# Kernel optimization log

Hardware: AMD Instinct MI355X
Metric: run time of the kernel (lower is better)

The kernel has to match this reference:

```python
import jax, jax.numpy as jnp
import numpy as np

N, H = 8192, 128  # nodes, hidden_dim


def setup_inputs() -> dict:
    key = jax.random.key(0)
    ks = jax.random.split(key, 5)
    X = jax.random.normal(ks[0], (N, H), dtype=jnp.float32)
    adj = jax.random.uniform(ks[1], (N, N), dtype=jnp.float32)
    W1 = jax.random.normal(ks[2], (H, H), dtype=jnp.float32) / np.sqrt(H).astype(np.float32)
    b1 = jnp.zeros((H,), jnp.float32)
    W2 = jax.random.normal(ks[3], (H, H), dtype=jnp.float32) / np.sqrt(H).astype(np.float32)
    b2 = jnp.zeros((H,), jnp.float32)
    a = jax.random.normal(ks[4], (2 * H, 1), dtype=jnp.float32) * 0.1
    return {"X": X, "adj": adj, "W1": W1, "b1": b1, "W2": W2, "b2": b2, "a": a}


def reference(X, adj, W1, b1, W2, b2, a):
    n = X.shape[0]
    leaky = jax.nn.leaky_relu  # negative_slope = 0.01, matches torch defaults

    # --- GCN diffusion: A_hat = A + I, symmetric normalization, 3 hops ---
    A_hat = adj + jnp.eye(n, dtype=adj.dtype)
    dinv_sqrt = jax.lax.rsqrt(A_hat.sum(axis=1))
    A_norm = dinv_sqrt[:, None] * A_hat * dinv_sqrt[None, :]
    hA = A_norm @ X
    hA2 = A_norm @ hA
    hA3 = A_norm @ hA2
    hA, hA2, hA3 = leaky(hA), leaky(hA2), leaky(hA3)

    # --- scattering diffusion: lazy walk P = 0.5*(I + A D^-1), wavelets ---
    deg = adj.sum(axis=1)
    AD = adj / deg[None, :]  # A @ D^{-1} (column-normalized)

    def P(v):
        return 0.5 * (v + AD @ v)

    px = P(X)
    p2x = P(px)
    p3x = P(p2x)
    p4x = P(p3x)
    # moment = 1 -> |.|**1
    s1 = jnp.abs(X - px)      # Psi_1 = I - P
    s2 = jnp.abs(px - p2x)    # Psi_2 = P - P^2
    s3 = jnp.abs(p2x - p4x)   # Psi_3 = P^2 - P^4

    # --- 6-way attention fusion ---
    h_all = jnp.stack([hA, hA2, hA3, s1, s2, s3], axis=1)         # [N,6,H]
    h_rep = jnp.broadcast_to(X[:, None, :], h_all.shape)          # [N,6,H]
    a_input = jnp.concatenate([h_rep, h_all], axis=-1)            # [N,6,2H]
    e = jnp.einsum('nsk,ko->ns', jax.nn.relu(a_input), a)         # [N,6]
    attn = jax.nn.softmax(e, axis=1)                              # [N,6]
    h_prime = jnp.mean(attn[:, :, None] * h_all, axis=1)          # [N,H]

    # --- output MLP (Withgres=False, so gres layer is skipped) ---
    out = leaky(h_prime @ W1.T + b1)
    out = leaky(out @ W2.T + b2)
    return out
```

## Files before the change

### kernel.cpp

```cpp
#include <hip/hip_runtime.h>

typedef unsigned short ushort_t;
typedef unsigned int   uint_t;
typedef int   i32x4 __attribute__((ext_vector_type(4)));

typedef __attribute__((address_space(3))) void lds_void_t;
typedef __attribute__((address_space(1))) void gbl_void_t;

#define NN 8192
#define HH 128
#define KS 8
#define KLEN 1024
#define NTQ 16

__device__ __forceinline__ ushort_t f2bf(float x) {
    uint_t u = __float_as_uint(x);
    u += 0x7fffu + ((u >> 16) & 1u);
    return (ushort_t)(u >> 16);
}
__device__ __forceinline__ float bf2f(uint_t lo16) { return __uint_as_float(lo16 << 16); }
__device__ __forceinline__ float leaky(float x) { return x > 0.f ? x : 0.01f * x; }

__global__ __launch_bounds__(256) void conv_rowsum(const float* __restrict__ adj,
    char* __restrict__ adjq, float* __restrict__ s, float* __restrict__ rinv)
{
    const int i = blockIdx.x;
    const float4* arow = (const float4*)(adj + ((size_t)i << 13));
    uint_t* brow = (uint_t*)(adjq + ((size_t)i << 13));
    float partial = 0.f;
    for (int t = threadIdx.x; t < 2048; t += 256) {
        const float4 v = arow[t];
        partial += (v.x + v.y) + (v.z + v.w);
        const uint_t q0 = (uint_t)__float2int_rn(v.x * 127.f);
        const uint_t q1 = (uint_t)__float2int_rn(v.y * 127.f);
        const uint_t q2 = (uint_t)__float2int_rn(v.z * 127.f);
        const uint_t q3 = (uint_t)__float2int_rn(v.w * 127.f);
        brow[t] = q0 | (q1 << 8) | (q2 << 16) | (q3 << 24);
    }
    #pragma unroll
    for (int off = 32; off; off >>= 1) partial += __shfl_xor(partial, off);
    __shared__ float ps[4];
    if ((threadIdx.x & 63) == 0) ps[threadIdx.x >> 6] = partial;
    __syncthreads();
    if (threadIdx.x == 0) {
        const float tot = (ps[0] + ps[1]) + (ps[2] + ps[3]);
        s[i]    = rsqrtf(tot + 1.0f);
        rinv[i] = 1.0f / tot;
    }
}

__global__ __launch_bounds__(256) void preMax(const float* __restrict__ u,
    const float* __restrict__ v, const float* __restrict__ s, const float* __restrict__ rinv,
    float* __restrict__ cmax)
{
    const int j0 = (blockIdx.x & 127) << 6;
    const int c0 = (blockIdx.x >> 7) << 6;
    __shared__ uint_t cm[64];
    if (threadIdx.x < 64) cm[threadIdx.x] = 0;
    __syncthreads();
    const int tx = threadIdx.x & 63;
    const int ty = threadIdx.x >> 6;
    float m = 0.f;
    #pragma unroll
    for (int rr = 0; rr < 16; ++rr) {
        const int j = j0 + ty + (rr << 2);
        const int c = c0 + tx;
        const float val = (c < 128) ? s[j] * u[((size_t)j << 7) + c]
                                    : rinv[j] * v[((size_t)j << 7) + (c - 128)];
        m = fmaxf(m, fabsf(val));
    }
    atomicMax(&cm[tx], __float_as_uint(m));
    __syncthreads();
    if (threadIdx.x < 64)
        atomicMax((uint_t*)&cmax[c0 + threadIdx.x], cm[threadIdx.x]);
}

__global__ __launch_bounds__(256) void preQ(const float* __restrict__ u,
    const float* __restrict__ v, const float* __restrict__ s, const float* __restrict__ rinv,
    const float* __restrict__ cmax, char* __restrict__ Bi8, float* __restrict__ dq)
{
    const int j0 = (blockIdx.x & 127) << 6;
    const int c0 = (blockIdx.x >> 7) << 6;
    __shared__ float tile[64][65];
    const int tx = threadIdx.x & 63;
    const int ty = threadIdx.x >> 6;
    #pragma unroll
    for (int rr = 0; rr < 16; ++rr) {
        const int jl = ty + (rr << 2);
        const int j = j0 + jl;
        const int c = c0 + tx;
        tile[jl][tx] = (c < 128) ? s[j] * u[((size_t)j << 7) + c]
                                 : rinv[j] * v[((size_t)j << 7) + (c - 128)];
    }
    __syncthreads();
    const int cl = threadIdx.x & 63;
    const int jq = threadIdx.x >> 6;
    const float cmv = cmax[c0 + cl];
    const float rs = cmv > 0.f ? 127.f / cmv : 0.f;
    uint_t w4[4];
    #pragma unroll
    for (int g = 0; g < 4; ++g) {
        uint_t wv = 0;
        #pragma unroll
        for (int b = 0; b < 4; ++b) {
            int q = __float2int_rn(tile[(jq << 4) + (g << 2) + b][cl] * rs);
            q = q > 127 ? 127 : (q < -127 ? -127 : q);
            wv |= ((uint_t)(q & 0xff)) << (8 * b);
        }
        w4[g] = wv;
    }
    uint4 st; st.x = w4[0]; st.y = w4[1]; st.z = w4[2]; st.w = w4[3];
    *(uint4*)(Bi8 + ((size_t)(c0 + cl) << 13) + j0 + (jq << 4)) = st;
    if ((blockIdx.x & 127) == 0 && threadIdx.x < 64)
        dq[c0 + threadIdx.x] = cmax[c0 + threadIdx.x] * (1.f / 16129.f);
}

#define WAITB(S) do {                                         \
    asm volatile("s_waitcnt " S ::: "memory");                \
    __builtin_amdgcn_sched_barrier(0);                        \
    __builtin_amdgcn_s_barrier();                             \
    __builtin_amdgcn_sched_barrier(0);                        \
} while (0)

__global__ __launch_bounds__(512, 2) void gemm_i8(const char* __restrict__ A,
    const char* __restrict__ Bt, ushort_t* __restrict__ Yb)
{
    __shared__ char lds[4 * 32768];
    const int bid = blockIdx.x;
    const int mb = bid & 31;
    const int ks = bid >> 5;
    const size_t mBase = (size_t)mb * 256;
    const int tid = threadIdx.x;
    const int w = tid >> 6, l = tid & 63;
    const int wr = w >> 2, wc = w & 3;
    const int frow = l & 15, fk = l >> 4;
    const int fsl = ((fk ^ ((frow >> 1) & 3)) << 4);
    const int srow = l >> 2;
    const int skoff = (((l & 3) ^ ((l >> 3) & 3)) << 4);
    const int kBeg = ks << 10;

    i32x4 acc[8][4] = {};

    auto STAGE = [&](int t) {
        const int k0 = kBeg + (t << 6);
        char* base = &lds[(t & 3) << 15];
        #pragma unroll
        for (int q = 0; q < 2; ++q) {
            const int c = (w << 1) + q;
            const int row = (c << 4) + srow;
            __builtin_amdgcn_global_load_lds(
                (const gbl_void_t*)(A + ((mBase + row) << 13) + k0 + skoff),
                (lds_void_t*)(base + (c << 10)), 16, 0, 0);
            __builtin_amdgcn_global_load_lds(
                (const gbl_void_t*)(Bt + ((size_t)row << 13) + k0 + skoff),
                (lds_void_t*)(base + 16384 + (c << 10)), 16, 0, 0);
        }
    };
    auto COMPUTE = [&](int T) {
        const char* buf = &lds[(T & 3) << 15];
        i32x4 av[8], bv[4];
        #pragma unroll
        for (int mi = 0; mi < 8; ++mi) {
            const int row = (wr << 7) + (mi << 4) + frow;
            av[mi] = *(const i32x4*)(buf + (row << 6) + fsl);
        }
        #pragma unroll
        for (int ni = 0; ni < 4; ++ni) {
            const int col = (wc << 6) + (ni << 4) + frow;
            bv[ni] = *(const i32x4*)(buf + 16384 + (col << 6) + fsl);
        }
        __builtin_amdgcn_s_setprio(1);
        #pragma unroll
        for (int mi = 0; mi < 8; ++mi)
            #pragma unroll
            for (int ni = 0; ni < 4; ++ni)
                acc[mi][ni] = __builtin_amdgcn_mfma_i32_16x16x64_i8(
                    av[mi], bv[ni], acc[mi][ni], 0, 0, 0);
        __builtin_amdgcn_s_setprio(0);
    };

    STAGE(0); STAGE(1); STAGE(2);
    #pragma unroll 1
    for (int T = 0; T < NTQ - 3; ++T) {
        WAITB("vmcnt(8)");
        STAGE(T + 3);
        COMPUTE(T);
    }
    WAITB("vmcnt(8)"); COMPUTE(NTQ - 3);
    WAITB("vmcnt(4)"); COMPUTE(NTQ - 2);
    WAITB("vmcnt(0)"); COMPUTE(NTQ - 1);
    __syncthreads();

    ushort_t* Cs = (ushort_t*)lds;
    const int orow = (l >> 4) << 2;
    const int ocol = l & 15;
    #pragma unroll
    for (int mi = 0; mi < 8; ++mi) {
        #pragma unroll
        for (int ni = 0; ni < 4; ++ni) {
            const int rl = (wr << 7) + (mi << 4) + orow;
            const int cl = (wc << 6) + (ni << 4) + ocol;
            #pragma unroll
            for (int r = 0; r < 4; ++r)
                Cs[(rl + r) * 256 + cl] = f2bf((float)acc[mi][ni][r]);
        }
    }
    __syncthreads();
    const size_t sliceBase = ((size_t)ks * NN + mBase) * 256;
    #pragma unroll
    for (int p = 0; p < 16; ++p) {
        const int idx16 = (p << 9) + tid;
        const int row   = idx16 >> 5;
        const int c16   = idx16 & 31;
        const uint4 v = *(const uint4*)(&Cs[(row << 8) + (c16 << 3)]);
        *(uint4*)(Yb + sliceBase + (size_t)row * 256 + (c16 << 3)) = v;
    }
}

__global__ __launch_bounds__(256, 2) void gemm_half_i8(const char* __restrict__ A,
    const char* __restrict__ Bt, ushort_t* __restrict__ Yb, int nbOff, int nbCount)
{
    __shared__ char lds[2 * 24576];
    const int bid  = blockIdx.x;
    const int mb   = bid & 31;
    const int rest = bid >> 5;
    const int nb   = nbOff + (rest % nbCount);
    const int ks   = rest / nbCount;
    const size_t mBase = (size_t)mb * 256;
    const size_t nBase = (size_t)nb * 128;
    const int tid = threadIdx.x;
    const int w = tid >> 6, l = tid & 63;
    const int wr = w >> 1, wc = w & 1;
    const int frow = l & 15, fk = l >> 4;
    const int fsl = ((fk ^ ((frow >> 1) & 3)) << 4);
    const int srow = l >> 2;
    const int skoff = (((l & 3) ^ ((l >> 3) & 3)) << 4);
    const int kBeg = ks << 10;

    i32x4 acc[8][4] = {};

    auto STAGE = [&](int t) {
        const int k0 = kBeg + (t << 6);
        char* base = &lds[(t & 1) * 24576];
        #pragma unroll
        for (int q = 0; q < 4; ++q) {
            const int c = (w << 2) + q;
            const int row = (c << 4) + srow;
            __builtin_amdgcn_global_load_lds(
                (const gbl_void_t*)(A + ((mBase + row) << 13) + k0 + skoff),
                (lds_void_t*)(base + (c << 10)), 16, 0, 0);
        }
        #pragma unroll
        for (int q = 0; q < 2; ++q) {
            const int c = (w << 1) + q;
            const int row = (c << 4) + srow;
            __builtin_amdgcn_global_load_lds(
                (const gbl_void_t*)(Bt + ((nBase + row) << 13) + k0 + skoff),
                (lds_void_t*)(base + 16384 + (c << 10)), 16, 0, 0);
        }
    };

    STAGE(0);
    __syncthreads();
    #pragma unroll 1
    for (int T = 0; T < NTQ; ++T) {
        if (T + 1 < NTQ) STAGE(T + 1);
        const char* buf = &lds[(T & 1) * 24576];
        i32x4 av[8], bv[4];
        #pragma unroll
        for (int mi = 0; mi < 8; ++mi) {
            const int row = (wr << 7) + (mi << 4) + frow;
            av[mi] = *(const i32x4*)(buf + (row << 6) + fsl);
        }
        #pragma unroll
        for (int ni = 0; ni < 4; ++ni) {
            const int col = (wc << 6) + (ni << 4) + frow;
            bv[ni] = *(const i32x4*)(buf + 16384 + (col << 6) + fsl);
        }
        __builtin_amdgcn_s_setprio(1);
        #pragma unroll
        for (int mi = 0; mi < 8; ++mi)
            #pragma unroll
            for (int ni = 0; ni < 4; ++ni)
                acc[mi][ni] = __builtin_amdgcn_mfma_i32_16x16x64_i8(
                    av[mi], bv[ni], acc[mi][ni], 0, 0, 0);
        __builtin_amdgcn_s_setprio(0);
        __syncthreads();
    }

    const int orow = (l >> 4) << 2;
    const int ocol = l & 15;
    const size_t sliceBase = ((size_t)ks * NN + mBase) * 256 + nBase;
    #pragma unroll
    for (int p = 0; p < 2; ++p) {
        __syncthreads();
        ushort_t* Cs = (ushort_t*)lds;
        #pragma unroll
        for (int mi = 0; mi < 4; ++mi) {
            #pragma unroll
            for (int ni = 0; ni < 4; ++ni) {
                const int rl = (wr << 6) + (mi << 4) + orow;
                const int cl = (wc << 6) + (ni << 4) + ocol;
                #pragma unroll
                for (int r = 0; r < 4; ++r)
                    Cs[(rl + r) * 128 + cl] = f2bf((float)acc[(p << 2) + mi][ni][r]);
            }
        }
        __syncthreads();
        #pragma unroll
        for (int pp = 0; pp < 8; ++pp) {
            const int idx16 = (pp << 8) + tid;
            const int lrow  = idx16 >> 4;
            const int c16   = idx16 & 15;
            const int rowIn = ((lrow >> 6) << 7) + (p << 6) + (lrow & 63);
            const uint4 v = *(const uint4*)(&Cs[(lrow << 7) + (c16 << 3)]);
            *(uint4*)(Yb + sliceBase + (size_t)rowIn * 256 + (c16 << 3)) = v;
        }
    }
}

__global__ __launch_bounds__(256) void reduce_post(const ushort_t* __restrict__ Yb,
    const float* __restrict__ u, const float* __restrict__ v,
    const float* __restrict__ s, const float* __restrict__ rinv,
    float* __restrict__ hop_out, float* __restrict__ walk_out,
    const float* __restrict__ dq, float* __restrict__ cmaxN, int c0Off)
{
    const int j0 = (blockIdx.x & 127) << 6;
    const int c0 = ((blockIdx.x >> 7) + c0Off) << 6;
    const bool hop = (c0 < 128);
    if (hop && hop_out == nullptr) return;
    __shared__ uint_t cm[64];
    if (cmaxN && threadIdx.x < 64) cm[threadIdx.x] = 0;
    if (cmaxN) __syncthreads();
    const int cg = threadIdx.x & 15;
    const int jr = threadIdx.x >> 4;
    const size_t SL = (size_t)NN * 256;
    const float4 dqv = ((const float4*)dq)[(c0 >> 2) + cg];
    float lm0 = 0.f, lm1 = 0.f, lm2 = 0.f, lm3 = 0.f;
    #pragma unroll
    for (int it = 0; it < 4; ++it) {
        const int jl = jr + (it << 4);
        const int j  = j0 + jl;
        const int c  = c0 + (cg << 2);
        const ushort_t* p = Yb + ((size_t)j << 8) + c;
        float e0 = 0.f, e1 = 0.f, e2 = 0.f, e3 = 0.f;
        #pragma unroll
        for (int kss = 0; kss < KS; ++kss) {
            const uint2 q = *(const uint2*)(p + kss * SL);
            e0 += bf2f(q.x & 0xffffu);
            e1 += __uint_as_float(q.x & 0xffff0000u);
            e2 += bf2f(q.y & 0xffffu);
            e3 += __uint_as_float(q.y & 0xffff0000u);
        }
        e0 *= dqv.x; e1 *= dqv.y; e2 *= dqv.z; e3 *= dqv.w;
        float4 o; float scale;
        if (hop) {
            const float si = s[j], si2 = si * si;
            const float4 uu = ((const float4*)u)[((size_t)j << 5) + (c >> 2)];
            o.x = si * e0 + si2 * uu.x;  o.y = si * e1 + si2 * uu.y;
            o.z = si * e2 + si2 * uu.z;  o.w = si * e3 + si2 * uu.w;
            ((float4*)hop_out)[((size_t)j << 5) + (c >> 2)] = o;
            scale = si;
        } else {
            const int cw = c - 128;
            const float4 vv = ((const float4*)v)[((size_t)j << 5) + (cw >> 2)];
            o.x = 0.5f * (vv.x + e0);  o.y = 0.5f * (vv.y + e1);
            o.z = 0.5f * (vv.z + e2);  o.w = 0.5f * (vv.w + e3);
            ((float4*)walk_out)[((size_t)j << 5) + (cw >> 2)] = o;
            scale = rinv[j];
        }
        if (cmaxN) {
            lm0 = fmaxf(lm0, fabsf(scale * o.x));
            lm1 = fmaxf(lm1, fabsf(scale * o.y));
            lm2 = fmaxf(lm2, fabsf(scale * o.z));
            lm3 = fmaxf(lm3, fabsf(scale * o.w));
        }
    }
    if (cmaxN) {
        atomicMax(&cm[(cg << 2) + 0], __float_as_uint(lm0));
        atomicMax(&cm[(cg << 2) + 1], __float_as_uint(lm1));
        atomicMax(&cm[(cg << 2) + 2], __float_as_uint(lm2));
        atomicMax(&cm[(cg << 2) + 3], __float_as_uint(lm3));
        __syncthreads();
        if (threadIdx.x < 64)
            atomicMax((uint_t*)&cmaxN[c0 + threadIdx.x], cm[threadIdx.x]);
    }
}

__global__ __launch_bounds__(256) void fuse_attn(const float* __restrict__ X,
    const float* __restrict__ hA, const float* __restrict__ hA2, const float* __restrict__ hA3,
    const float* __restrict__ px, const float* __restrict__ p2x, const float* __restrict__ p4x,
    const float* __restrict__ a, float* __restrict__ hp)
{
    const int w = threadIdx.x >> 6, l = threadIdx.x & 63;
    const size_t i = (size_t)blockIdx.x * 4 + w;
    const size_t base = i << 7;
    float f[6][2];
    float e[6] = {0.f, 0.f, 0.f, 0.f, 0.f, 0.f};
    #pragma unroll
    for (int h = 0; h < 2; ++h) {
        const int k = l + (h << 6);
        const float a2 = a[128 + k];
        const float x   = X[base + k];
        const float t1  = leaky(hA [base + k]);
        const float t2  = leaky(hA2[base + k]);
        const float t3  = leaky(hA3[base + k]);
        const float pk  = px [base + k];
        const float p2k = p2x[base + k];
        const float p4k = p4x[base + k];
        const float s1 = fabsf(x - pk);
        const float s2 = fabsf(pk - p2k);
        const float s3 = fabsf(p2k - p4k);
        f[0][h] = t1; f[1][h] = t2; f[2][h] = t3;
        f[3][h] = s1; f[4][h] = s2; f[5][h] = s3;
        e[0] += fmaxf(t1, 0.f) * a2;
        e[1] += fmaxf(t2, 0.f) * a2;
        e[2] += fmaxf(t3, 0.f) * a2;
        e[3] += s1 * a2;
        e[4] += s2 * a2;
        e[5] += s3 * a2;
    }
    #pragma unroll
    for (int ss = 0; ss < 6; ++ss) {
        #pragma unroll
        for (int off = 32; off; off >>= 1) e[ss] += __shfl_xor(e[ss], off);
    }
    float mx = e[0];
    #pragma unroll
    for (int ss = 1; ss < 6; ++ss) mx = fmaxf(mx, e[ss]);
    float at[6], sum = 0.f;
    #pragma unroll
    for (int ss = 0; ss < 6; ++ss) { at[ss] = expf(e[ss] - mx); sum += at[ss]; }
    const float inv = 1.f / (6.f * sum);
    #pragma unroll
    for (int h = 0; h < 2; ++h) {
        float o = 0.f;
        #pragma unroll
        for (int ss = 0; ss < 6; ++ss) o += at[ss] * f[ss][h];
        hp[base + l + (h << 6)] = o * inv;
    }
}

__global__ __launch_bounds__(256) void mlp(const float* __restrict__ Hm,
    const float* __restrict__ W, const float* __restrict__ b, float* __restrict__ out)
{
    __shared__ float Ws[128 * 140];
    __shared__ float Hs[16 * 140];
    const int node0 = blockIdx.x << 4;
    for (int rr = 0; rr < 64; ++rr) {
        const int idx = rr * 256 + threadIdx.x;
        Ws[(idx >> 7) * 140 + (idx & 127)] = W[idx];
    }
    #pragma unroll
    for (int rr = 0; rr < 8; ++rr) {
        const int idx = rr * 256 + threadIdx.x;
        Hs[(idx >> 7) * 140 + (idx & 127)] = Hm[((size_t)node0 << 7) + idx];
    }
    __syncthreads();
    const int c = threadIdx.x & 15;
    const int n = threadIdx.x >> 4;
    float acc[8] = {};
    for (int k4 = 0; k4 < 32; ++k4) {
        const float4 h4 = *(const float4*)(&Hs[n * 140 + (k4 << 2)]);
        #pragma unroll
        for (int r = 0; r < 8; ++r) {
            const float4 w4 = *(const float4*)(&Ws[(c + (r << 4)) * 140 + (k4 << 2)]);
            acc[r] += h4.x * w4.x + h4.y * w4.y + h4.z * w4.z + h4.w * w4.w;
        }
    }
    const size_t obase = ((size_t)(node0 + n)) << 7;
    #pragma unroll
    for (int r = 0; r < 8; ++r) {
        const int o = c + (r << 4);
        out[obase + o] = leaky(acc[r] + b[o]);
    }
}

extern "C" void kernel_launch(void* const* d_in, const int* in_sizes, int n_in,
                              void* d_out, int out_size, void* d_ws, size_t ws_size,
                              hipStream_t stream)
{
    const float* X   = (const float*)d_in[0];
    const float* adj = (const float*)d_in[1];
    const float* W1  = (const float*)d_in[2];
    const float* b1  = (const float*)d_in[3];
    const float* W2  = (const float*)d_in[4];
    const float* b2  = (const float*)d_in[5];
    const float* a   = (const float*)d_in[6];
    float* out = (float*)d_out;

    char* ws = (char*)d_ws;
    char*     adjq = ws;
    char*     Bi8  = ws + 67108864ull;
    ushort_t* Yb   = (ushort_t*)(ws + 69206016ull);
    float* hA  = (float*)(ws + 102760448ull);
    float* hA2 = hA  + 1048576;
    float* hA3 = hA2 + 1048576;
    float* px  = hA3 + 1048576;
    float* p2x = px  + 1048576;
    float* p3x = p2x + 1048576;
    float* p4x = p3x + 1048576;
    float* sbuf  = p4x + 1048576;
    float* rinvb = sbuf + 8192;
    float* cmaxb = rinvb + 8192;
    float* dq    = cmaxb + 1024;
    float* cmax1 = cmaxb, *cmax2 = cmaxb + 256, *cmax3 = cmaxb + 512, *cmax4 = cmaxb + 768;
    float* hp   = (float*)Yb;
    float* out1 = (float*)(ws + 69206016ull + 4194304ull);

    hipMemsetAsync(cmaxb, 0, 4096, stream);
    conv_rowsum<<<8192, 256, 0, stream>>>(adj, adjq, sbuf, rinvb);

    preMax<<<512, 256, 0, stream>>>(X, X, sbuf, rinvb, cmax1);
    preQ  <<<512, 256, 0, stream>>>(X, X, sbuf, rinvb, cmax1, Bi8, dq);
    gemm_i8<<<256, 512, 0, stream>>>(adjq, Bi8, Yb);
    reduce_post<<<512, 256, 0, stream>>>(Yb, X, X, sbuf, rinvb,
                                         hA, px, dq, cmax2, 0);
    preQ  <<<512, 256, 0, stream>>>(hA, px, sbuf, rinvb, cmax2, Bi8, dq);
    gemm_i8<<<256, 512, 0, stream>>>(adjq, Bi8, Yb);
    reduce_post<<<512, 256, 0, stream>>>(Yb, hA, px, sbuf, rinvb,
                                         hA2, p2x, dq, cmax3, 0);
    preQ  <<<512, 256, 0, stream>>>(hA2, p2x, sbuf, rinvb, cmax3, Bi8, dq);
    gemm_i8<<<256, 512, 0, stream>>>(adjq, Bi8, Yb);
    reduce_post<<<512, 256, 0, stream>>>(Yb, hA2, p2x, sbuf, rinvb,
                                         hA3, p3x, dq, cmax4, 0);
    preQ  <<<512, 256, 0, stream>>>(hA3, p3x, sbuf, rinvb, cmax4, Bi8, dq);
    gemm_half_i8<<<256, 256, 0, stream>>>(adjq, Bi8, Yb, 1, 1);
    reduce_post<<<256, 256, 0, stream>>>(Yb, nullptr, p3x, sbuf, rinvb,
                                         nullptr, p4x, dq, nullptr, 2);

    fuse_attn<<<2048, 256, 0, stream>>>(X, hA, hA2, hA3, px, p2x, p4x, a, hp);
    mlp<<<512, 256, 0, stream>>>(hp, W1, b1, out1);
    mlp<<<512, 256, 0, stream>>>(out1, W2, b2, out);
}
```

Before: 267.2 us.

## Fuse quantization into reduce via grid barrier and merge attention with MLP

Merges the column-max and quantize passes into one kernel using a software grid barrier, so each reduce step also quantizes the next GEMM's operand in place. Fuses the attention-fusion kernel with both MLP layers into one kernel that keeps intermediates in shared memory. Replaces the memset by zeroing inside conv_rowsum. This removes several kernel launches and global round-trips of activations. The grid barrier depends on all 512 blocks being co-resident, which risks deadlock if occupancy is insufficient, and it makes reduceQuant read dq and write the next dq through the same buffer.

```diff
diff --git a/kernel.cpp b/kernel.cpp
--- a/kernel.cpp
+++ b/kernel.cpp
@@ -12,6 +12,7 @@
 #define KS 8
 #define KLEN 1024
 #define NTQ 16
+#define NBAR 512u
 
 __device__ __forceinline__ ushort_t f2bf(float x) {
     uint_t u = __float_as_uint(x);
@@ -21,10 +22,31 @@
 __device__ __forceinline__ float bf2f(uint_t lo16) { return __uint_as_float(lo16 << 16); }
 __device__ __forceinline__ float leaky(float x) { return x > 0.f ? x : 0.01f * x; }
 
+__device__ __forceinline__ void grid_barrier(uint_t* ctr) {
+    __threadfence();
+    __syncthreads();
+    if (threadIdx.x == 0) {
+        __hip_atomic_fetch_add(ctr, 1u, __ATOMIC_ACQ_REL, __HIP_MEMORY_SCOPE_AGENT);
+        while (__hip_atomic_load(ctr, __ATOMIC_ACQUIRE, __HIP_MEMORY_SCOPE_AGENT) < NBAR)
+            __builtin_amdgcn_s_sleep(2);
+    }
+    __syncthreads();
+}
+__device__ __forceinline__ float cmax_read(const float* p) {
+    return __uint_as_float(__hip_atomic_load((const uint_t*)p,
+        __ATOMIC_RELAXED, __HIP_MEMORY_SCOPE_AGENT));
+}
+
 __global__ __launch_bounds__(256) void conv_rowsum(const float* __restrict__ adj,
-    char* __restrict__ adjq, float* __restrict__ s, float* __restrict__ rinv)
+    char* __restrict__ adjq, float* __restrict__ s, float* __restrict__ rinv,
+    float* __restrict__ zbase)
 {
     const int i = blockIdx.x;
+    if (i == 0) {
+        const float4 z{0.f, 0.f, 0.f, 0.f};
+        ((float4*)zbase)[threadIdx.x] = z;
+        if (threadIdx.x < 128) ((float4*)zbase)[256 + threadIdx.x] = z;
+    }
     const float4* arow = (const float4*)(adj + ((size_t)i << 13));
     uint_t* brow = (uint_t*)(adjq + ((size_t)i << 13));
     float partial = 0.f;
@@ -49,53 +71,36 @@
     }
 }
 
-__global__ __launch_bounds__(256) void preMax(const float* __restrict__ u,
-    const float* __restrict__ v, const float* __restrict__ s, const float* __restrict__ rinv,
-    float* __restrict__ cmax)
-{
-    const int j0 = (blockIdx.x & 127) << 6;
-    const int c0 = (blockIdx.x >> 7) << 6;
-    __shared__ uint_t cm[64];
-    if (threadIdx.x < 64) cm[threadIdx.x] = 0;
-    __syncthreads();
-    const int tx = threadIdx.x & 63;
-    const int ty = threadIdx.x >> 6;
-    float m = 0.f;
-    #pragma unroll
-    for (int rr = 0; rr < 16; ++rr) {
-        const int j = j0 + ty + (rr << 2);
-        const int c = c0 + tx;
-        const float val = (c < 128) ? s[j] * u[((size_t)j << 7) + c]
-                                    : rinv[j] * v[((size_t)j << 7) + (c - 128)];
-        m = fmaxf(m, fabsf(val));
-    }
-    atomicMax(&cm[tx], __float_as_uint(m));
-    __syncthreads();
-    if (threadIdx.x < 64)
-        atomicMax((uint_t*)&cmax[c0 + threadIdx.x], cm[threadIdx.x]);
-}
-
-__global__ __launch_bounds__(256) void preQ(const float* __restrict__ u,
-    const float* __restrict__ v, const float* __restrict__ s, const float* __restrict__ rinv,
-    const float* __restrict__ cmax, char* __restrict__ Bi8, float* __restrict__ dq)
+__global__ __launch_bounds__(256) void quantX(const float* __restrict__ X,
+    const float* __restrict__ s, const float* __restrict__ rinv,
+    float* __restrict__ cmax, char* __restrict__ Bi8, float* __restrict__ dq,
+    uint_t* __restrict__ ctr)
 {
     const int j0 = (blockIdx.x & 127) << 6;
     const int c0 = (blockIdx.x >> 7) << 6;
     __shared__ float tile[64][65];
-    const int tx = threadIdx.x & 63;
-    const int ty = threadIdx.x >> 6;
+    __shared__ uint_t cm[64];
+    const int tid = threadIdx.x;
+    if (tid < 64) cm[tid] = 0;
+    __syncthreads();
+    const int tx = tid & 63, ty = tid >> 6;
+    float m = 0.f;
     #pragma unroll
     for (int rr = 0; rr < 16; ++rr) {
         const int jl = ty + (rr << 2);
         const int j = j0 + jl;
         const int c = c0 + tx;
-        tile[jl][tx] = (c < 128) ? s[j] * u[((size_t)j << 7) + c]
-                                 : rinv[j] * v[((size_t)j << 7) + (c - 128)];
-    }
-    __syncthreads();
-    const int cl = threadIdx.x & 63;
-    const int jq = threadIdx.x >> 6;
-    const float cmv = cmax[c0 + cl];
+        const float val = (c < 128) ? s[j] * X[((size_t)j << 7) + c]
+                                    : rinv[j] * X[((size_t)j << 7) + (c - 128)];
+        tile[jl][tx] = val;
+        m = fmaxf(m, fabsf(val));
+    }
+    atomicMax(&cm[tx], __float_as_uint(m));
+    __syncthreads();
+    if (tid < 64) atomicMax((uint_t*)&cmax[c0 + tid], cm[tid]);
+    grid_barrier(ctr);
+    const int cl = tid & 63, jq = tid >> 6;
+    const float cmv = cmax_read(&cmax[c0 + cl]);
     const float rs = cmv > 0.f ? 127.f / cmv : 0.f;
     uint_t w4[4];
     #pragma unroll
@@ -111,8 +116,8 @@
     }
     uint4 st; st.x = w4[0]; st.y = w4[1]; st.z = w4[2]; st.w = w4[3];
     *(uint4*)(Bi8 + ((size_t)(c0 + cl) << 13) + j0 + (jq << 4)) = st;
-    if ((blockIdx.x & 127) == 0 && threadIdx.x < 64)
-        dq[c0 + threadIdx.x] = cmax[c0 + threadIdx.x] * (1.f / 16129.f);
+    if ((blockIdx.x & 127) == 0 && tid < 64)
+        dq[c0 + tid] = cmv * (1.f / 16129.f);
 }
 
 #define WAITB(S) do {                                         \
@@ -319,21 +324,22 @@
     }
 }
 
-__global__ __launch_bounds__(256) void reduce_post(const ushort_t* __restrict__ Yb,
+__global__ __launch_bounds__(256) void reduceQuant(const ushort_t* __restrict__ Yb,
     const float* __restrict__ u, const float* __restrict__ v,
     const float* __restrict__ s, const float* __restrict__ rinv,
     float* __restrict__ hop_out, float* __restrict__ walk_out,
-    const float* __restrict__ dq, float* __restrict__ cmaxN, int c0Off)
+    const float* __restrict__ dq, float* __restrict__ cmaxN,
+    char* __restrict__ Bi8, float* __restrict__ dqN, uint_t* __restrict__ ctr)
 {
     const int j0 = (blockIdx.x & 127) << 6;
-    const int c0 = ((blockIdx.x >> 7) + c0Off) << 6;
+    const int c0 = (blockIdx.x >> 7) << 6;
     const bool hop = (c0 < 128);
-    if (hop && hop_out == nullptr) return;
+    __shared__ float tile[64][65];
     __shared__ uint_t cm[64];
-    if (cmaxN && threadIdx.x < 64) cm[threadIdx.x] = 0;
-    if (cmaxN) __syncthreads();
-    const int cg = threadIdx.x & 15;
-    const int jr = threadIdx.x >> 4;
+    const int tid = threadIdx.x;
+    if (tid < 64) cm[tid] = 0;
+    __syncthreads();
+    const int cg = tid & 15, jr = tid >> 4;
     const size_t SL = (size_t)NN * 256;
     const float4 dqv = ((const float4*)dq)[(c0 >> 2) + cg];
     float lm0 = 0.f, lm1 = 0.f, lm2 = 0.f, lm3 = 0.f;
@@ -369,37 +375,97 @@
             ((float4*)walk_out)[((size_t)j << 5) + (cw >> 2)] = o;
             scale = rinv[j];
         }
-        if (cmaxN) {
-            lm0 = fmaxf(lm0, fabsf(scale * o.x));
-            lm1 = fmaxf(lm1, fabsf(scale * o.y));
-            lm2 = fmaxf(lm2, fabsf(scale * o.z));
-            lm3 = fmaxf(lm3, fabsf(scale * o.w));
-        }
-    }
-    if (cmaxN) {
-        atomicMax(&cm[(cg << 2) + 0], __float_as_uint(lm0));
-        atomicMax(&cm[(cg << 2) + 1], __float_as_uint(lm1));
-        atomicMax(&cm[(cg << 2) + 2], __float_as_uint(lm2));
-        atomicMax(&cm[(cg << 2) + 3], __float_as_uint(lm3));
-        __syncthreads();
-        if (threadIdx.x < 64)
-            atomicMax((uint_t*)&cmaxN[c0 + threadIdx.x], cm[threadIdx.x]);
-    }
-}
-
-__global__ __launch_bounds__(256) void fuse_attn(const float* __restrict__ X,
+        const float b0 = scale * o.x, b1 = scale * o.y;
+        const float b2 = scale * o.z, b3 = scale * o.w;
+        const int clb = cg << 2;
+        tile[jl][clb + 0] = b0;  tile[jl][clb + 1] = b1;
+        tile[jl][clb + 2] = b2;  tile[jl][clb + 3] = b3;
+        lm0 = fmaxf(lm0, fabsf(b0));  lm1 = fmaxf(lm1, fabsf(b1));
+        lm2 = fmaxf(lm2, fabsf(b2));  lm3 = fmaxf(lm3, fabsf(b3));
+    }
+    atomicMax(&cm[(cg << 2) + 0], __float_as_uint(lm0));
+    atomicMax(&cm[(cg << 2) + 1], __float_as_uint(lm1));
+    atomicMax(&cm[(cg << 2) + 2], __float_as_uint(lm2));
+    atomicMax(&cm[(cg << 2) + 3], __float_as_uint(lm3));
+    __syncthreads();
+    if (tid < 64) atomicMax((uint_t*)&cmaxN[c0 + tid], cm[tid]);
+    grid_barrier(ctr);
+    const int cl = tid & 63, jq = tid >> 6;
+    const float cmv = cmax_read(&cmaxN[c0 + cl]);
+    const float rs = cmv > 0.f ? 127.f / cmv : 0.f;
+    uint_t w4[4];
+    #pragma unroll
+    for (int g = 0; g < 4; ++g) {
+        uint_t wv = 0;
+        #pragma unroll
+        for (int b = 0; b < 4; ++b) {
+            int q = __float2int_rn(tile[(jq << 4) + (g << 2) + b][cl] * rs);
+            q = q > 127 ? 127 : (q < -127 ? -127 : q);
+            wv |= ((uint_t)(q & 0xff)) << (8 * b);
+        }
+        w4[g] = wv;
+    }
+    uint4 st; st.x = w4[0]; st.y = w4[1]; st.z = w4[2]; st.w = w4[3];
+    *(uint4*)(Bi8 + ((size_t)(c0 + cl) << 13) + j0 + (jq << 4)) = st;
+    if ((blockIdx.x & 127) == 0 && tid < 64)
+        dqN[c0 + tid] = cmv * (1.f / 16129.f);
+}
+
+__global__ __launch_bounds__(256) void reduce4(const ushort_t* __restrict__ Yb,
+    const float* __restrict__ v, const float* __restrict__ dq,
+    float* __restrict__ walk_out)
+{
+    const int j0 = (blockIdx.x & 127) << 6;
+    const int c0 = ((blockIdx.x >> 7) + 2) << 6;
+    const int cg = threadIdx.x & 15, jr = threadIdx.x >> 4;
+    const size_t SL = (size_t)NN * 256;
+    const float4 dqv = ((const float4*)dq)[(c0 >> 2) + cg];
+    #pragma unroll
+    for (int it = 0; it < 4; ++it) {
+        const int jl = jr + (it << 4);
+        const int j  = j0 + jl;
+        const int c  = c0 + (cg << 2);
+        const ushort_t* p = Yb + ((size_t)j << 8) + c;
+        float e0 = 0.f, e1 = 0.f, e2 = 0.f, e3 = 0.f;
+        #pragma unroll
+        for (int kss = 0; kss < KS; ++kss) {
+            const uint2 q = *(const uint2*)(p + kss * SL);
+            e0 += bf2f(q.x & 0xffffu);
+            e1 += __uint_as_float(q.x & 0xffff0000u);
+            e2 += bf2f(q.y & 0xffffu);
+            e3 += __uint_as_float(q.y & 0xffff0000u);
+        }
+        const int cw = c - 128;
+        const float4 vv = ((const float4*)v)[((size_t)j << 5) + (cw >> 2)];
+        float4 o;
+        o.x = 0.5f * (vv.x + e0 * dqv.x);  o.y = 0.5f * (vv.y + e1 * dqv.y);
+        o.z = 0.5f * (vv.z + e2 * dqv.z);  o.w = 0.5f * (vv.w + e3 * dqv.w);
+        ((float4*)walk_out)[((size_t)j << 5) + (cw >> 2)] = o;
+    }
+}
+
+__global__ __launch_bounds__(256) void attn_mlp(const float* __restrict__ X,
     const float* __restrict__ hA, const float* __restrict__ hA2, const float* __restrict__ hA3,
     const float* __restrict__ px, const float* __restrict__ p2x, const float* __restrict__ p4x,
-    const float* __restrict__ a, float* __restrict__ hp)
-{
-    const int w = threadIdx.x >> 6, l = threadIdx.x & 63;
-    const size_t i = (size_t)blockIdx.x * 4 + w;
-    const size_t base = i << 7;
-    float f[6][2];
+    const float* __restrict__ a, const float* __restrict__ W1, const float* __restrict__ b1,
+    const float* __restrict__ W2, const float* __restrict__ b2, float* __restrict__ out)
+{
+    __shared__ float Ws[128 * 132];
+    __shared__ float Hs[16 * 132];
+    const int tid = threadIdx.x;
+    const int node0 = blockIdx.x << 4;
+    const int n = tid >> 4, c = tid & 15;
+    for (int rr = 0; rr < 64; ++rr) {
+        const int idx = rr * 256 + tid;
+        Ws[(idx >> 7) * 132 + (idx & 127)] = W1[idx];
+    }
+    const size_t base = ((size_t)(node0 + n)) << 7;
+    const int k0 = c << 3;
+    float f[6][8];
     float e[6] = {0.f, 0.f, 0.f, 0.f, 0.f, 0.f};
     #pragma unroll
-    for (int h = 0; h < 2; ++h) {
-        const int k = l + (h << 6);
+    for (int h = 0; h < 8; ++h) {
+        const int k = k0 + h;
         const float a2 = a[128 + k];
         const float x   = X[base + k];
         const float t1  = leaky(hA [base + k]);
@@ -423,7 +489,7 @@
     #pragma unroll
     for (int ss = 0; ss < 6; ++ss) {
         #pragma unroll
-        for (int off = 32; off; off >>= 1) e[ss] += __shfl_xor(e[ss], off);
+        for (int off = 8; off; off >>= 1) e[ss] += __shfl_xor(e[ss], off);
     }
     float mx = e[0];
     #pragma unroll
@@ -433,46 +499,46 @@
     for (int ss = 0; ss < 6; ++ss) { at[ss] = expf(e[ss] - mx); sum += at[ss]; }
     const float inv = 1.f / (6.f * sum);
     #pragma unroll
-    for (int h = 0; h < 2; ++h) {
+    for (int h = 0; h < 8; ++h) {
         float o = 0.f;
         #pragma unroll
         for (int ss = 0; ss < 6; ++ss) o += at[ss] * f[ss][h];
-        hp[base + l + (h << 6)] = o * inv;
-    }
-}
-
-__global__ __launch_bounds__(256) void mlp(const float* __restrict__ Hm,
-    const float* __restrict__ W, const float* __restrict__ b, float* __restrict__ out)
-{
-    __shared__ float Ws[128 * 140];
-    __shared__ float Hs[16 * 140];
-    const int node0 = blockIdx.x << 4;
-    for (int rr = 0; rr < 64; ++rr) {
-        const int idx = rr * 256 + threadIdx.x;
-        Ws[(idx >> 7) * 140 + (idx & 127)] = W[idx];
-    }
-    #pragma unroll
-    for (int rr = 0; rr < 8; ++rr) {
-        const int idx = rr * 256 + threadIdx.x;
-        Hs[(idx >> 7) * 140 + (idx & 127)] = Hm[((size_t)node0 << 7) + idx];
-    }
-    __syncthreads();
-    const int c = threadIdx.x & 15;
-    const int n = threadIdx.x >> 4;
+        Hs[n * 132 + k0 + h] = o * inv;
+    }
+    __syncthreads();
     float acc[8] = {};
     for (int k4 = 0; k4 < 32; ++k4) {
-        const float4 h4 = *(const float4*)(&Hs[n * 140 + (k4 << 2)]);
+        const float4 h4 = *(const float4*)(&Hs[n * 132 + (k4 << 2)]);
         #pragma unroll
         for (int r = 0; r < 8; ++r) {
-            const float4 w4 = *(const float4*)(&Ws[(c + (r << 4)) * 140 + (k4 << 2)]);
+            const float4 w4 = *(const float4*)(&Ws[(c + (r << 4)) * 132 + (k4 << 2)]);
             acc[r] += h4.x * w4.x + h4.y * w4.y + h4.z * w4.z + h4.w * w4.w;
         }
     }
-    const size_t obase = ((size_t)(node0 + n)) << 7;
+    __syncthreads();
     #pragma unroll
     for (int r = 0; r < 8; ++r) {
         const int o = c + (r << 4);
-        out[obase + o] = leaky(acc[r] + b[o]);
+        Hs[n * 132 + o] = leaky(acc[r] + b1[o]);
+    }
+    for (int rr = 0; rr < 64; ++rr) {
+        const int idx = rr * 256 + tid;
+        Ws[(idx >> 7) * 132 + (idx & 127)] = W2[idx];
+    }
+    __syncthreads();
+    float acc2[8] = {};
+    for (int k4 = 0; k4 < 32; ++k4) {
+        const float4 h4 = *(const float4*)(&Hs[n * 132 + (k4 << 2)]);
+        #pragma unroll
+        for (int r = 0; r < 8; ++r) {
+            const float4 w4 = *(const float4*)(&Ws[(c + (r << 4)) * 132 + (k4 << 2)]);
+            acc2[r] += h4.x * w4.x + h4.y * w4.y + h4.z * w4.z + h4.w * w4.w;
+        }
+    }
+    #pragma unroll
+    for (int r = 0; r < 8; ++r) {
+        const int o = c + (r << 4);
+        out[base + o] = leaky(acc2[r] + b2[o]);
     }
 }
 
@@ -504,32 +570,24 @@
     float* rinvb = sbuf + 8192;
     float* cmaxb = rinvb + 8192;
     float* dq    = cmaxb + 1024;
+    uint_t* ctr  = (uint_t*)(cmaxb + 1280);
     float* cmax1 = cmaxb, *cmax2 = cmaxb + 256, *cmax3 = cmaxb + 512, *cmax4 = cmaxb + 768;
-    float* hp   = (float*)Yb;
-    float* out1 = (float*)(ws + 69206016ull + 4194304ull);
-
-    hipMemsetAsync(cmaxb, 0, 4096, stream);
-    conv_rowsum<<<8192, 256, 0, stream>>>(adj, adjq, sbuf, rinvb);
-
-    preMax<<<512, 256, 0, stream>>>(X, X, sbuf, rinvb, cmax1);
-    preQ  <<<512, 256, 0, stream>>>(X, X, sbuf, rinvb, cmax1, Bi8, dq);
+
+    conv_rowsum<<<8192, 256, 0, stream>>>(adj, adjq, sbuf, rinvb, cmaxb);
+
+    quantX<<<512, 256, 0, stream>>>(X, sbuf, rinvb, cmax1, Bi8, dq, ctr + 0);
     gemm_i8<<<256, 512, 0, stream>>>(adjq, Bi8, Yb);
-    reduce_post<<<512, 256, 0, stream>>>(Yb, X, X, sbuf, rinvb,
-                                         hA, px, dq, cmax2, 0);
-    preQ  <<<512, 256, 0, stream>>>(hA, px, sbuf, rinvb, cmax2, Bi8, dq);
+    reduceQuant<<<512, 256, 0, stream>>>(Yb, X, X, sbuf, rinvb,
+                                         hA, px, dq, cmax2, Bi8, dq, ctr + 1);
     gemm_i8<<<256, 512, 0, stream>>>(adjq, Bi8, Yb);
-    reduce_post<<<512, 256, 0, stream>>>(Yb, hA, px, sbuf, rinvb,
-                                         hA2, p2x, dq, cmax3, 0);
-    preQ  <<<512, 256, 0, stream>>>(hA2, p2x, sbuf, rinvb, cmax3, Bi8, dq);
+    reduceQuant<<<512, 256, 0, stream>>>(Yb, hA, px, sbuf, rinvb,
+                                         hA2, p2x, dq, cmax3, Bi8, dq, ctr + 2);
     gemm_i8<<<256, 512, 0, stream>>>(adjq, Bi8, Yb);
-    reduce_post<<<512, 256, 0, stream>>>(Yb, hA2, p2x, sbuf, rinvb,
-                                         hA3, p3x, dq, cmax4, 0);
-    preQ  <<<512, 256, 0, stream>>>(hA3, p3x, sbuf, rinvb, cmax4, Bi8, dq);
+    reduceQuant<<<512, 256, 0, stream>>>(Yb, hA2, p2x, sbuf, rinvb,
+                                         hA3, p3x, dq, cmax4, Bi8, dq, ctr + 3);
     gemm_half_i8<<<256, 256, 0, stream>>>(adjq, Bi8, Yb, 1, 1);
-    reduce_post<<<256, 256, 0, stream>>>(Yb, nullptr, p3x, sbuf, rinvb,
-                                         nullptr, p4x, dq, nullptr, 2);
-
-    fuse_attn<<<2048, 256, 0, stream>>>(X, hA, hA2, hA3, px, p2x, p4x, a, hp);
-    mlp<<<512, 256, 0, stream>>>(hp, W1, b1, out1);
-    mlp<<<512, 256, 0, stream>>>(out1, W2, b2, out);
-}
+    reduce4<<<256, 256, 0, stream>>>(Yb, p3x, dq, p4x);
+
+    attn_mlp<<<512, 256, 0, stream>>>(X, hA, hA2, hA3, px, p2x, p4x, a,
+                                      W1, b1, W2, b2, out);
+}
```

After: 460.4 us. +72.3%, slower.
